# Optimization experiments

Measured on AMD Instinct MI355X. Metric: run time of the kernel, lower is better.

## Reference

```python
import jax, jax.numpy as jnp
import numpy as np

V, M, E, H = 20000, 32, 128, 4      # vocab, max news per word, embed dim, heads
N, L, C = 8192, 64, 128             # num news, max sent len, cnn out channels
KS = (3, 4, 5)


def setup_inputs() -> dict:
    key = jax.random.key(0)
    ks = jax.random.split(key, 12)
    s = 0.02
    return {
        "word2news": jax.random.randint(ks[0], (V, M), 0, N),
        "word2news_len": jax.random.randint(ks[1], (V,), 0, M),
        "news_words": jax.random.randint(ks[2], (N, L), 0, V),
        "news_embed_table": jax.random.normal(ks[3], (N, E), jnp.float32) * s,
        "in_proj_w": jax.random.normal(ks[4], (3 * E, E), jnp.float32) * s,
        "in_proj_b": jnp.zeros((3 * E,), jnp.float32),
        "out_proj_w": jax.random.normal(ks[5], (E, E), jnp.float32) * s,
        "out_proj_b": jnp.zeros((E,), jnp.float32),
        "conv_w3": jax.random.normal(ks[6], (C, E, 3), jnp.float32) * s,
        "conv_b3": jnp.zeros((C,), jnp.float32),
        "conv_w4": jax.random.normal(ks[7], (C, E, 4), jnp.float32) * s,
        "conv_b4": jnp.zeros((C,), jnp.float32),
        "conv_w5": jax.random.normal(ks[8], (C, E, 5), jnp.float32) * s,
        "conv_b5": jnp.zeros((C,), jnp.float32),
        "fc_w": jax.random.normal(ks[9], (E, len(KS) * C), jnp.float32) * s,
        "fc_b": jnp.zeros((E,), jnp.float32),
    }


def _conv1d(x, w, b):
    # x: [N, E, L]  w: [C, E, k]  -> [N, C, L-k+1]
    y = jax.lax.conv_general_dilated(x, w, (1,), "VALID",
                                     dimension_numbers=("NCH", "OIH", "NCH"))
    return y + b[None, :, None]


def _word_embeds(word2news, word2news_len, table, in_w, in_b, out_w, out_b):
    # Batched version of the per-word loop: masked mean query + 1-query MHA.
    mask = jnp.arange(M)[None, :] < word2news_len[:, None]          # [V, M]
    ctx = table[word2news]                                           # [V, M, E]
    cnt = jnp.maximum(word2news_len, 1).astype(ctx.dtype)[:, None]
    q = jnp.sum(jnp.where(mask[:, :, None], ctx, 0.0), axis=1) / cnt  # [V, E]
    wq, wk, wv = jnp.split(in_w, 3, axis=0)
    bq, bk, bv = jnp.split(in_b, 3, axis=0)
    Dh = E // H
    qh = (q @ wq.T + bq).reshape(V, H, Dh)
    kh = (ctx @ wk.T + bk).reshape(V, M, H, Dh)
    vh = (ctx @ wv.T + bv).reshape(V, M, H, Dh)
    scores = jnp.einsum("vhd,vmhd->vhm", qh, kh) / jnp.sqrt(jnp.asarray(Dh, ctx.dtype))
    scores = jnp.where(mask[:, None, :], scores, -1e9)
    attn = jax.nn.softmax(scores, axis=-1)
    o = jnp.einsum("vhm,vmhd->vhd", attn, vh).reshape(V, E)
    o = o @ out_w.T + out_b
    # words with no news stay zero, matching the zeros-init table in torch
    return jnp.where((word2news_len > 0)[:, None], o, 0.0)            # [V, E]


def reference(word2news, word2news_len, news_words, news_embed_table,
              in_proj_w, in_proj_b, out_proj_w, out_proj_b,
              conv_w3, conv_b3, conv_w4, conv_b4, conv_w5, conv_b5,
              fc_w, fc_b):
    word_embeds = _word_embeds(word2news, word2news_len, news_embed_table,
                               in_proj_w, in_proj_b, out_proj_w, out_proj_b)
    doc = word_embeds[news_words]                 # [N, L, E]
    x = doc.transpose(0, 2, 1)                    # [N, E, L]
    pooled = [jnp.max(jax.nn.relu(_conv1d(x, w, b)), axis=2)
              for w, b in ((conv_w3, conv_b3), (conv_w4, conv_b4), (conv_w5, conv_b5))]
    feats = jnp.concatenate(pooled, axis=1)       # [N, 3*C]; dropout=identity (eval)
    return feats @ fc_w.T + fc_b                  # [N, E]
```

## Files before the change

kernel.cpp:

```cpp
#include <hip/hip_runtime.h>
#include <math.h>

#define V_WORDS 20000
#define MM 32
#define EE 128
#define HH 4
#define DHH 32
#define NN 8192
#define LL 64
#define CC 128

typedef short bf16x8 __attribute__((ext_vector_type(8)));
typedef float f32x4 __attribute__((ext_vector_type(4)));
typedef unsigned short u16;
typedef unsigned int u32;

__device__ __forceinline__ u16 f2bf(float x) {
    u32 u = __float_as_uint(x);
    u32 r = (u + 0x7FFFu + ((u >> 16) & 1u)) >> 16;
    return (u16)r;
}
__device__ __forceinline__ float bflo(u32 u) { return __uint_as_float(u << 16); }
__device__ __forceinline__ float bfhi(u32 u) { return __uint_as_float(u & 0xFFFF0000u); }

#if defined(__has_builtin)
#  if __has_builtin(__builtin_amdgcn_fdot2_f32_bf16)
#    define USE_BF16_DOT2 1
#  endif
#endif
#ifdef USE_BF16_DOT2
typedef __bf16 v2bf __attribute__((ext_vector_type(2)));
#endif

__device__ __forceinline__ float dot2bf(u32 a, u32 b, float c) {
#ifdef USE_BF16_DOT2
    return __builtin_amdgcn_fdot2_f32_bf16(
        __builtin_bit_cast(v2bf, a), __builtin_bit_cast(v2bf, b), c, false);
#else
    return c + bflo(a) * bflo(b) + bfhi(a) * bfhi(b);
#endif
}

__global__ __launch_bounds__(256)
void pack_weights(const float* __restrict__ w3,
                  const float* __restrict__ w4,
                  const float* __restrict__ w5,
                  u16* __restrict__ Bpack)
{
    const int s = blockIdx.x;
    const int t = threadIdx.x;
    const int lane = t & 63;

    const float* src;
    int K, sl;
    if (s < 12)      { src = w3; K = 3; sl = s; }
    else if (s < 28) { src = w4; K = 4; sl = s - 12; }
    else             { src = w5; K = 5; sl = s - 28; }
    const int j  = sl >> 2;
    const int e0 = (sl & 3) * 32;

    for (int nt = (t >> 6); nt < 8; nt += 4) {
        const int c = nt * 16 + (lane & 15);
        const int kb = (lane >> 4) * 8;
        u16 vals[8];
        #pragma unroll
        for (int i = 0; i < 8; ++i) {
            const int e = e0 + kb + i;
            vals[i] = f2bf(src[(c * EE + e) * K + j]);
        }
        u16* dst = Bpack + (((size_t)s * 8 + nt) * 64 + lane) * 8;
        *(bf16x8*)dst = *(const bf16x8*)vals;
    }
}

__global__ __launch_bounds__(256)
void kv_proj_kernel(const float* __restrict__ table,
                    const float* __restrict__ in_w,
                    const float* __restrict__ in_b,
                    u16* __restrict__ Kn16, u16* __restrict__ Vn16)
{
    const int n0 = blockIdx.x * 8;
    const int t = threadIdx.x;
    __shared__ float tbl[8][EE];
    {
        const int r = t >> 5, q4 = (t & 31) * 4;
        *(float4*)&tbl[r][q4] = *(const float4*)&table[(size_t)(n0 + r) * EE + q4];
    }
    __syncthreads();

    const int sel = t >> 7;
    const int i = t & 127;
    const float* w = in_w + (size_t)(sel + 1) * EE * EE + (size_t)i * EE;
    const float bias = in_b[(sel + 1) * EE + i];

    float acc[8];
    #pragma unroll
    for (int r = 0; r < 8; ++r) acc[r] = bias;
    for (int k = 0; k < EE; k += 4) {
        const float4 wv = *(const float4*)&w[k];
        #pragma unroll
        for (int r = 0; r < 8; ++r) {
            acc[r] += tbl[r][k]     * wv.x + tbl[r][k + 1] * wv.y
                    + tbl[r][k + 2] * wv.z + tbl[r][k + 3] * wv.w;
        }
    }
    u16* dst = sel ? Vn16 : Kn16;
    #pragma unroll
    for (int r = 0; r < 8; ++r) dst[(size_t)(n0 + r) * EE + i] = f2bf(acc[r]);
}

__global__ __launch_bounds__(384)
void kvqw_proj_kernel(const float* __restrict__ table,
                      const float* __restrict__ in_w,
                      const float* __restrict__ in_b,
                      const float* __restrict__ out_w,
                      const float* __restrict__ out_b,
                      u16* __restrict__ Qn16,
                      u16* __restrict__ Kn16,
                      u16* __restrict__ Wn16)
{
    const int n0 = blockIdx.x * 8;
    const int t = threadIdx.x;
    __shared__ float tbl[8][EE];
    __shared__ float vsh[8][EE];
    if (t < 256) {
        const int r = t >> 5, q4 = (t & 31) * 4;
        *(float4*)&tbl[r][q4] = *(const float4*)&table[(size_t)(n0 + r) * EE + q4];
    }
    __syncthreads();

    const int sel = t >> 7;
    const int i = t & 127;
    const float* w = in_w + (size_t)sel * EE * EE + (size_t)i * EE;
    const float bias = in_b[sel * EE + i];

    float acc[8];
    #pragma unroll
    for (int r = 0; r < 8; ++r) acc[r] = bias;
    for (int k = 0; k < EE; k += 4) {
        const float4 wv = *(const float4*)&w[k];
        #pragma unroll
        for (int r = 0; r < 8; ++r) {
            acc[r] += tbl[r][k]     * wv.x + tbl[r][k + 1] * wv.y
                    + tbl[r][k + 2] * wv.z + tbl[r][k + 3] * wv.w;
        }
    }
    if (sel == 0) {
        #pragma unroll
        for (int r = 0; r < 8; ++r) Qn16[(size_t)(n0 + r) * EE + i] = f2bf(acc[r]);
    } else if (sel == 1) {
        #pragma unroll
        for (int r = 0; r < 8; ++r) Kn16[(size_t)(n0 + r) * EE + i] = f2bf(acc[r]);
    } else {
        #pragma unroll
        for (int r = 0; r < 8; ++r) vsh[r][i] = acc[r];
    }
    __syncthreads();

    {
        const int g = t >> 7;
        const int r0 = g, r1 = g + 3, r2 = g + 6;
        const int r2c = (r2 < 8) ? r2 : 7;
        const float* wr = out_w + (size_t)i * EE;
        const float ob = out_b[i];
        float a0 = ob, a1 = ob, a2 = ob;
        #pragma unroll 4
        for (int k = 0; k < EE; k += 4) {
            const float4 wv = *(const float4*)&wr[k];
            a0 += vsh[r0][k]   * wv.x + vsh[r0][k+1] * wv.y
                + vsh[r0][k+2] * wv.z + vsh[r0][k+3] * wv.w;
            a1 += vsh[r1][k]   * wv.x + vsh[r1][k+1] * wv.y
                + vsh[r1][k+2] * wv.z + vsh[r1][k+3] * wv.w;
            a2 += vsh[r2c][k]   * wv.x + vsh[r2c][k+1] * wv.y
                + vsh[r2c][k+2] * wv.z + vsh[r2c][k+3] * wv.w;
        }
        Wn16[(size_t)(n0 + r0) * EE + i] = f2bf(a0);
        Wn16[(size_t)(n0 + r1) * EE + i] = f2bf(a1);
        if (r2 < 8) Wn16[(size_t)(n0 + r2) * EE + i] = f2bf(a2);
    }
}

#define WPB 8
__global__ __launch_bounds__(256, 3)
void word_attn_kernel(const int* __restrict__ word2news,
                      const int* __restrict__ word2news_len,
                      const float* __restrict__ table,
                      const float* __restrict__ in_w,
                      const float* __restrict__ in_b,
                      const float* __restrict__ out_w,
                      const float* __restrict__ out_b,
                      const u16* __restrict__ Kn16,
                      const u16* __restrict__ Vn16,
                      u16* __restrict__ we16)
{
    const int v0 = blockIdx.x * WPB;
    const int t = threadIdx.x;

    __shared__ int   rows[WPB][MM];
    __shared__ int   lenS[WPB];
    __shared__ float q[WPB][EE];
    __shared__ float qh[WPB][EE];
    __shared__ float attn[WPB][HH][MM];
    __shared__ float osh[WPB][EE];

    {
        const int w = t >> 5, m = t & 31;
        rows[w][m] = word2news[(size_t)(v0 + w) * MM + m];
        if (t < WPB) lenS[t] = word2news_len[v0 + t];
    }
    __syncthreads();

    {
        const int w = t >> 5, d0 = (t & 31) * 4;
        const int L = lenS[w];
        float4 a = {0.f, 0.f, 0.f, 0.f};
        #pragma unroll 4
        for (int m = 0; m < MM; ++m) {
            const float4 x = *(const float4*)&table[(size_t)rows[w][m] * EE + d0];
            if (m < L) { a.x += x.x; a.y += x.y; a.z += x.z; a.w += x.w; }
        }
        const float inv = (L > 0) ? 1.0f / (float)L : 0.0f;
        a.x *= inv; a.y *= inv; a.z *= inv; a.w *= inv;
        *(float4*)&q[w][d0] = a;
    }
    __syncthreads();

    {
        const int g = t >> 7, i = t & 127;
        const float* wr = in_w + (size_t)i * EE;
        float acc[4] = {0.f, 0.f, 0.f, 0.f};
        #pragma unroll 4
        for (int k = 0; k < EE; k += 4) {
            const float4 wv = *(const float4*)&wr[k];
            #pragma unroll
            for (int w4 = 0; w4 < 4; ++w4) {
                const float* qw = q[g * 4 + w4];
                acc[w4] += qw[k] * wv.x + qw[k + 1] * wv.y
                         + qw[k + 2] * wv.z + qw[k + 3] * wv.w;
            }
        }
        const float b = in_b[i];
        #pragma unroll
        for (int w4 = 0; w4 < 4; ++w4) qh[g * 4 + w4][i] = acc[w4] + b;
    }
    __syncthreads();

    {
        const int w = t >> 5, m = t & 31;
        const int L = lenS[w];
        float s[HH] = {-1e9f, -1e9f, -1e9f, -1e9f};
        if (m < L) {
            const uint4* kr = (const uint4*)(Kn16 + (size_t)rows[w][m] * EE);
            #pragma unroll 1
            for (int h = 0; h < HH; ++h) {
                float a = 0.f;
                #pragma unroll
                for (int k8 = 0; k8 < 4; ++k8) {
                    const uint4 u = kr[h * 4 + k8];
                    const float4 q0 = *(const float4*)&qh[w][h * 32 + k8 * 8];
                    const float4 q1 = *(const float4*)&qh[w][h * 32 + k8 * 8 + 4];
                    a += q0.x * bflo(u.x) + q0.y * bfhi(u.x)
                       + q0.z * bflo(u.y) + q0.w * bfhi(u.y)
                       + q1.x * bflo(u.z) + q1.y * bfhi(u.z)
                       + q1.z * bflo(u.w) + q1.w * bfhi(u.w);
                }
                s[h] = a * 0.17677669529663687f;
            }
        }
        #pragma unroll
        for (int h = 0; h < HH; ++h) {
            float mx = s[h];
            #pragma unroll
            for (int off = 16; off > 0; off >>= 1)
                mx = fmaxf(mx, __shfl_xor(mx, off, 32));
            const float ex = expf(s[h] - mx);
            float sum = ex;
            #pragma unroll
            for (int off = 16; off > 0; off >>= 1)
                sum += __shfl_xor(sum, off, 32);
            attn[w][h][m] = ex / sum;
        }
    }
    __syncthreads();

    {
        const int w = t >> 5, d0 = (t & 31) * 4;
        const int h = d0 >> 5;
        float4 a = {0.f, 0.f, 0.f, 0.f};
        #pragma unroll 4
        for (int m = 0; m < MM; ++m) {
            const float aw = attn[w][h][m];
            const u32* vr = (const u32*)(Vn16 + (size_t)rows[w][m] * EE + d0);
            const u32 u0 = vr[0], u1 = vr[1];
            a.x += aw * bflo(u0); a.y += aw * bfhi(u0);
            a.z += aw * bflo(u1); a.w += aw * bfhi(u1);
        }
        *(float4*)&osh[w][d0] = a;
    }
    __syncthreads();

    {
        const int g = t >> 7, i = t & 127;
        const float* wr = out_w + (size_t)i * EE;
        float acc[4] = {0.f, 0.f, 0.f, 0.f};
        #pragma unroll 4
        for (int k = 0; k < EE; k += 4) {
            const float4 wv = *(const float4*)&wr[k];
            #pragma unroll
            for (int w4 = 0; w4 < 4; ++w4) {
                const float* ow = osh[g * 4 + w4];
                acc[w4] += ow[k] * wv.x + ow[k + 1] * wv.y
                         + ow[k + 2] * wv.z + ow[k + 3] * wv.w;
            }
        }
        const float b = out_b[i];
        #pragma unroll
        for (int w4 = 0; w4 < 4; ++w4) {
            const int w = g * 4 + w4;
            we16[(size_t)(v0 + w) * EE + i] =
                (lenS[w] > 0) ? f2bf(acc[w4] + b) : (u16)0;
        }
    }
}

__global__ __launch_bounds__(256, 3)
void word_attn_wn(const int* __restrict__ word2news,
                  const int* __restrict__ word2news_len,
                  const u16* __restrict__ Qn16,
                  const u16* __restrict__ Kn16,
                  const u16* __restrict__ Wn16,
                  u16* __restrict__ we16)
{
    const int v0 = blockIdx.x * WPB;
    const int t = threadIdx.x;

    __shared__ int   rows[WPB][MM];
    __shared__ int   lenS[WPB];
    __shared__ __align__(16) u32 qhp[WPB][EE / 2];
    __shared__ float attn[WPB][HH][MM];

    {
        const int w = t >> 5, m = t & 31;
        rows[w][m] = word2news[(size_t)(v0 + w) * MM + m];
        if (t < WPB) lenS[t] = word2news_len[v0 + t];
    }
    __syncthreads();

    {
        const int w = t >> 5, d0 = (t & 31) * 4;
        const int L = lenS[w];
        float4 a = {0.f, 0.f, 0.f, 0.f};
        #pragma unroll 4
        for (int m = 0; m < L; ++m) {
            const uint2 u = *(const uint2*)(Qn16 + (size_t)rows[w][m] * EE + d0);
            a.x += bflo(u.x); a.y += bfhi(u.x);
            a.z += bflo(u.y); a.w += bfhi(u.y);
        }
        const float inv = (L > 0) ? 1.0f / (float)L : 0.0f;
        a.x *= inv; a.y *= inv; a.z *= inv; a.w *= inv;
        qhp[w][(d0 >> 1) + 0] = (u32)f2bf(a.x) | ((u32)f2bf(a.y) << 16);
        qhp[w][(d0 >> 1) + 1] = (u32)f2bf(a.z) | ((u32)f2bf(a.w) << 16);
    }
    __syncthreads();

    {
        const int w = t >> 5, m = t & 31;
        const int L = lenS[w];
        float s[HH] = {-1e9f, -1e9f, -1e9f, -1e9f};
        if (m < L) {
            const uint4* kr = (const uint4*)(Kn16 + (size_t)rows[w][m] * EE);
            const u32* qp = qhp[w];
            #pragma unroll
            for (int hp = 0; hp < 2; ++hp) {
                uint4 kq[8];
                #pragma unroll
                for (int q8 = 0; q8 < 8; ++q8) kq[q8] = kr[hp * 8 + q8];
                #pragma unroll
                for (int hl = 0; hl < 2; ++hl) {
                    const int h = hp * 2 + hl;
                    float a = 0.f;
                    #pragma unroll
                    for (int k8 = 0; k8 < 4; ++k8) {
                        const uint4 u  = kq[hl * 4 + k8];
                        const uint4 qq = *(const uint4*)&qp[h * 16 + k8 * 4];
                        a = dot2bf(u.x, qq.x, a);
                        a = dot2bf(u.y, qq.y, a);
                        a = dot2bf(u.z, qq.z, a);
                        a = dot2bf(u.w, qq.w, a);
                    }
                    s[h] = a * 0.17677669529663687f;
                }
            }
        }
        #pragma unroll
        for (int h = 0; h < HH; ++h) {
            float mx = s[h];
            #pragma unroll
            for (int off = 16; off > 0; off >>= 1)
                mx = fmaxf(mx, __shfl_xor(mx, off, 32));
            const float ex = expf(s[h] - mx);
            float sum = ex;
            #pragma unroll
            for (int off = 16; off > 0; off >>= 1)
                sum += __shfl_xor(sum, off, 32);
            attn[w][h][m] = ex / sum;
        }
    }
    __syncthreads();

    {
        const int w = t >> 5, d0 = (t & 31) * 4;
        const int h = d0 >> 5;
        const int L = lenS[w];
        float4 a = {0.f, 0.f, 0.f, 0.f};
        #pragma unroll 4
        for (int m = 0; m < L; ++m) {
            const float aw = attn[w][h][m];
            const uint2 u = *(const uint2*)(Wn16 + (size_t)rows[w][m] * EE + d0);
            a.x += aw * bflo(u.x); a.y += aw * bfhi(u.x);
            a.z += aw * bflo(u.y); a.w += aw * bfhi(u.y);
        }
        u32 lo = 0u, hi = 0u;
        if (L > 0) {
            lo = (u32)f2bf(a.x) | ((u32)f2bf(a.y) << 16);
            hi = (u32)f2bf(a.z) | ((u32)f2bf(a.w) << 16);
        }
        u32* dst = (u32*)(we16 + (size_t)(v0 + w) * EE + d0);
        dst[0] = lo; dst[1] = hi;
    }
}

#define DSTRIDE 136
#define DOCSZ   (68 * DSTRIDE)

template<int NSL, int SBASE, int NP>
__device__ __forceinline__ void conv_g2(const u16* __restrict__ lds,
                                        const u16* __restrict__ Bpack,
                                        const float* __restrict__ bk,
                                        int p, int nth, int l,
                                        float (&mxout)[4])
{
    f32x4 acc[4][4];
    #pragma unroll
    for (int mt = 0; mt < 4; ++mt)
        #pragma unroll
        for (int k = 0; k < 4; ++k)
            acc[mt][k] = (f32x4){0.f, 0.f, 0.f, 0.f};

    const int lm = l & 15;
    const int g  = l >> 4;
    const u16* bbase = Bpack + ((size_t)SBASE * 8 + nth * 4) * 512 + l * 8;
    const u16* abase = lds + (size_t)p * DOCSZ;

    #pragma unroll 2
    for (int s = 0; s < NSL; ++s) {
        const int j  = s >> 2;
        const int e0 = (s & 3) * 32;

        bf16x8 b[4];
        #pragma unroll
        for (int k = 0; k < 4; ++k)
            b[k] = *(const bf16x8*)(bbase + s * 4096 + k * 512);

        const u16* arow = abase + (lm + j) * DSTRIDE + e0 + g * 8;
        bf16x8 a[4];
        #pragma unroll
        for (int mt = 0; mt < 4; ++mt)
            a[mt] = *(const bf16x8*)(arow + mt * (16 * DSTRIDE));

        #pragma unroll
        for (int mt = 0; mt < 4; ++mt)
            #pragma unroll
            for (int k = 0; k < 4; ++k)
                acc[mt][k] = __builtin_amdgcn_mfma_f32_16x16x32_bf16(a[mt], b[k], acc[mt][k], 0, 0, 0);
    }

    #pragma unroll
    for (int k = 0; k < 4; ++k) {
        const int c = nth * 64 + k * 16 + lm;
        const float bias = bk[c];
        float mx = 0.0f;
        #pragma unroll
        for (int mt = 0; mt < 4; ++mt) {
            #pragma unroll
            for (int r = 0; r < 4; ++r) {
                const int pos = 16 * mt + g * 4 + r;
                const float y = fmaxf(acc[mt][k][r] + bias, 0.0f);
                if (pos < NP) mx = fmaxf(mx, y);
            }
        }
        mx = fmaxf(mx, __shfl_xor(mx, 16));
        mx = fmaxf(mx, __shfl_xor(mx, 32));
        mxout[k] = mx;
    }
}

__global__ __launch_bounds__(512, 4)
void news_kernel(const int* __restrict__ news_words,
                 const u16* __restrict__ we16,
                 const u16* __restrict__ Bpack,
                 const float* __restrict__ b3,
                 const float* __restrict__ b4,
                 const float* __restrict__ b5,
                 const float* __restrict__ fcw, const float* __restrict__ fcb,
                 float* __restrict__ out)
{
    const int n0 = blockIdx.x * 4;
    const int t = threadIdx.x;
    const int w = t >> 6, l = t & 63;
    const int p = w >> 1, nth = w & 1;

    __shared__ u16 lds[4 * DOCSZ];
    __shared__ int rows[4 * LL];

    if (t < 4 * LL) rows[t] = news_words[(size_t)n0 * LL + t];
    __syncthreads();

    {
        const uint4* weU = (const uint4*)we16;
        uint4* ldsU = (uint4*)lds;
        for (int idx = t; idx < 4096; idx += 512) {
            const int d = idx >> 10, rem = idx & 1023;
            const int row = rem >> 4, c4 = rem & 15;
            ldsU[d * 1156 + row * 17 + c4] = weU[(size_t)rows[d * 64 + row] * 16 + c4];
        }
        if (t < 256) {
            const int d = t >> 6, rem = t & 63;
            const int row = 64 + (rem >> 4), c4 = rem & 15;
            ldsU[d * 1156 + row * 17 + c4] = (uint4){0u, 0u, 0u, 0u};
        }
    }
    __syncthreads();

    float m3[4], m4[4], m5[4];
    conv_g2<12,  0, 62>(lds, Bpack, b3, p, nth, l, m3);
    conv_g2<16, 12, 61>(lds, Bpack, b4, p, nth, l, m4);
    conv_g2<20, 28, 60>(lds, Bpack, b5, p, nth, l, m5);
    __syncthreads();

    float* feats = (float*)lds;
    if ((l >> 4) == 0) {
        const int lm = l & 15;
        #pragma unroll
        for (int k = 0; k < 4; ++k) {
            const int c = nth * 64 + k * 16 + lm;
            feats[p * 384 +   0 + c] = m3[k];
            feats[p * 384 + 128 + c] = m4[k];
            feats[p * 384 + 256 + c] = m5[k];
        }
    }
    __syncthreads();

    if (t < 128) {
        const float4* wr4 = (const float4*)(fcw + (size_t)t * (3 * CC));
        float a0 = fcb[t], a1 = a0, a2 = a0, a3 = a0;
        for (int f4 = 0; f4 < 96; ++f4) {
            const float4 wv = wr4[f4];
            const float4 x0 = *(const float4*)&feats[0 * 384 + f4 * 4];
            const float4 x1 = *(const float4*)&feats[1 * 384 + f4 * 4];
            const float4 x2 = *(const float4*)&feats[2 * 384 + f4 * 4];
            const float4 x3 = *(const float4*)&feats[3 * 384 + f4 * 4];
            a0 += x0.x * wv.x + x0.y * wv.y + x0.z * wv.z + x0.w * wv.w;
            a1 += x1.x * wv.x + x1.y * wv.y + x1.z * wv.z + x1.w * wv.w;
            a2 += x2.x * wv.x + x2.y * wv.y + x2.z * wv.z + x2.w * wv.w;
            a3 += x3.x * wv.x + x3.y * wv.y + x3.z * wv.z + x3.w * wv.w;
        }
        out[(size_t)(n0 + 0) * EE + t] = a0;
        out[(size_t)(n0 + 1) * EE + t] = a1;
        out[(size_t)(n0 + 2) * EE + t] = a2;
        out[(size_t)(n0 + 3) * EE + t] = a3;
    }
}

extern "C" void kernel_launch(void* const* d_in, const int* in_sizes, int n_in,
                              void* d_out, int out_size, void* d_ws, size_t ws_size,
                              hipStream_t stream)
{
    const int*   word2news     = (const int*)d_in[0];
    const int*   word2news_len = (const int*)d_in[1];
    const int*   news_words    = (const int*)d_in[2];
    const float* table         = (const float*)d_in[3];
    const float* in_w          = (const float*)d_in[4];
    const float* in_b          = (const float*)d_in[5];
    const float* out_w         = (const float*)d_in[6];
    const float* out_b         = (const float*)d_in[7];
    const float* w3            = (const float*)d_in[8];
    const float* b3            = (const float*)d_in[9];
    const float* w4            = (const float*)d_in[10];
    const float* b4            = (const float*)d_in[11];
    const float* w5            = (const float*)d_in[12];
    const float* b5            = (const float*)d_in[13];
    const float* fcw           = (const float*)d_in[14];
    const float* fcb           = (const float*)d_in[15];

    float* out = (float*)d_out;
    u16* base  = (u16*)d_ws;
    u16* we16  = base;
    u16* Bpack = base + 2560000;
    u16* Kn16  = base + 2756608;
    u16* Wn16  = base + 3805184;
    u16* Qn16  = base + 4853760;
    const size_t need_qn = (size_t)(4853760 + 1048576) * 2;

    pack_weights<<<48, 256, 0, stream>>>(w3, w4, w5, Bpack);

    if (ws_size >= need_qn) {
        kvqw_proj_kernel<<<NN / 8, 384, 0, stream>>>(table, in_w, in_b,
                                                     out_w, out_b,
                                                     Qn16, Kn16, Wn16);
        word_attn_wn<<<V_WORDS / WPB, 256, 0, stream>>>(
            word2news, word2news_len, Qn16, Kn16, Wn16, we16);
    } else {
        kv_proj_kernel<<<NN / 8, 256, 0, stream>>>(table, in_w, in_b, Kn16, Wn16);
        word_attn_kernel<<<V_WORDS / WPB, 256, 0, stream>>>(
            word2news, word2news_len, table, in_w, in_b, out_w, out_b,
            Kn16, Wn16, we16);
    }

    news_kernel<<<NN / 4, 512, 0, stream>>>(
        news_words, we16, Bpack, b3, b4, b5, fcw, fcb, out);
}
```

Baseline: 364.5 us.

## Assign 64 threads per word in attention kernel, splitting rows and heads

```diff
diff --git a/kernel.cpp b/kernel.cpp
--- a/kernel.cpp
+++ b/kernel.cpp
@@ -323,6 +323,7 @@
     }
 }
 
+#define WPW 4
 __global__ __launch_bounds__(256, 3)
 void word_attn_wn(const int* __restrict__ word2news,
                   const int* __restrict__ word2news_len,
@@ -331,102 +332,114 @@
                   const u16* __restrict__ Wn16,
                   u16* __restrict__ we16)
 {
-    const int v0 = blockIdx.x * WPB;
+    const int v0 = blockIdx.x * WPW;
     const int t = threadIdx.x;
-
-    __shared__ int   rows[WPB][MM];
-    __shared__ int   lenS[WPB];
-    __shared__ __align__(16) u32 qhp[WPB][EE / 2];
-    __shared__ float attn[WPB][HH][MM];
-
-    {
-        const int w = t >> 5, m = t & 31;
-        rows[w][m] = word2news[(size_t)(v0 + w) * MM + m];
-        if (t < WPB) lenS[t] = word2news_len[v0 + t];
-    }
-    __syncthreads();
-
-    {
-        const int w = t >> 5, d0 = (t & 31) * 4;
-        const int L = lenS[w];
+    const int w   = t >> 6;
+    const int l   = t & 63;
+    const int h2  = l >> 5;
+    const int m32 = l & 31;
+
+    __shared__ int   rows[WPW][MM];
+    __shared__ int   lenS[WPW];
+    __shared__ __align__(16) u32 qhp[WPW][EE / 2];
+    __shared__ float attn[WPW][HH][MM];
+
+    {
+        if (t < WPW * MM) rows[t >> 5][t & 31] = word2news[(size_t)v0 * MM + t];
+        if (t < WPW) lenS[t] = word2news_len[v0 + t];
+    }
+    __syncthreads();
+
+    const int L  = lenS[w];
+    const int d0 = m32 * 4;
+
+    {
         float4 a = {0.f, 0.f, 0.f, 0.f};
         #pragma unroll 4
-        for (int m = 0; m < L; ++m) {
-            const uint2 u = *(const uint2*)(Qn16 + (size_t)rows[w][m] * EE + d0);
-            a.x += bflo(u.x); a.y += bfhi(u.x);
-            a.z += bflo(u.y); a.w += bfhi(u.y);
-        }
+        for (int mm = 0; mm < L; mm += 2) {
+            const int ri = mm + h2;
+            if (ri < L) {
+                const uint2 u = *(const uint2*)(Qn16 + (size_t)rows[w][ri] * EE + d0);
+                a.x += bflo(u.x); a.y += bfhi(u.x);
+                a.z += bflo(u.y); a.w += bfhi(u.y);
+            }
+        }
+        a.x += __shfl_xor(a.x, 32);
+        a.y += __shfl_xor(a.y, 32);
+        a.z += __shfl_xor(a.z, 32);
+        a.w += __shfl_xor(a.w, 32);
         const float inv = (L > 0) ? 1.0f / (float)L : 0.0f;
-        a.x *= inv; a.y *= inv; a.z *= inv; a.w *= inv;
-        qhp[w][(d0 >> 1) + 0] = (u32)f2bf(a.x) | ((u32)f2bf(a.y) << 16);
-        qhp[w][(d0 >> 1) + 1] = (u32)f2bf(a.z) | ((u32)f2bf(a.w) << 16);
-    }
-    __syncthreads();
-
-    {
-        const int w = t >> 5, m = t & 31;
-        const int L = lenS[w];
-        float s[HH] = {-1e9f, -1e9f, -1e9f, -1e9f};
-        if (m < L) {
-            const uint4* kr = (const uint4*)(Kn16 + (size_t)rows[w][m] * EE);
+        if (h2 == 0) {
+            qhp[w][(d0 >> 1) + 0] = (u32)f2bf(a.x * inv) | ((u32)f2bf(a.y * inv) << 16);
+            qhp[w][(d0 >> 1) + 1] = (u32)f2bf(a.z * inv) | ((u32)f2bf(a.w * inv) << 16);
+        }
+    }
+    __syncthreads();
+
+    {
+        float s[2] = {-1e9f, -1e9f};
+        if (m32 < L) {
+            const uint4* kr = (const uint4*)(Kn16 + (size_t)rows[w][m32] * EE);
+            uint4 kq[8];
+            #pragma unroll
+            for (int i = 0; i < 8; ++i) kq[i] = kr[h2 * 8 + i];
             const u32* qp = qhp[w];
             #pragma unroll
-            for (int hp = 0; hp < 2; ++hp) {
-                uint4 kq[8];
+            for (int hl = 0; hl < 2; ++hl) {
+                const int h = h2 * 2 + hl;
+                float a = 0.f;
                 #pragma unroll
-                for (int q8 = 0; q8 < 8; ++q8) kq[q8] = kr[hp * 8 + q8];
-                #pragma unroll
-                for (int hl = 0; hl < 2; ++hl) {
-                    const int h = hp * 2 + hl;
-                    float a = 0.f;
-                    #pragma unroll
-                    for (int k8 = 0; k8 < 4; ++k8) {
-                        const uint4 u  = kq[hl * 4 + k8];
-                        const uint4 qq = *(const uint4*)&qp[h * 16 + k8 * 4];
-                        a = dot2bf(u.x, qq.x, a);
-                        a = dot2bf(u.y, qq.y, a);
-                        a = dot2bf(u.z, qq.z, a);
-                        a = dot2bf(u.w, qq.w, a);
-                    }
-                    s[h] = a * 0.17677669529663687f;
+                for (int k8 = 0; k8 < 4; ++k8) {
+                    const uint4 u  = kq[hl * 4 + k8];
+                    const uint4 qq = *(const uint4*)&qp[h * 16 + k8 * 4];
+                    a = dot2bf(u.x, qq.x, a);
+                    a = dot2bf(u.y, qq.y, a);
+                    a = dot2bf(u.z, qq.z, a);
+                    a = dot2bf(u.w, qq.w, a);
                 }
+                s[hl] = a * 0.17677669529663687f;
             }
         }
         #pragma unroll
-        for (int h = 0; h < HH; ++h) {
-            float mx = s[h];
+        for (int hl = 0; hl < 2; ++hl) {
+            float mx = s[hl];
             #pragma unroll
             for (int off = 16; off > 0; off >>= 1)
                 mx = fmaxf(mx, __shfl_xor(mx, off, 32));
-            const float ex = expf(s[h] - mx);
+            const float ex = __expf(s[hl] - mx);
             float sum = ex;
             #pragma unroll
             for (int off = 16; off > 0; off >>= 1)
                 sum += __shfl_xor(sum, off, 32);
-            attn[w][h][m] = ex / sum;
-        }
-    }
-    __syncthreads();
-
-    {
-        const int w = t >> 5, d0 = (t & 31) * 4;
-        const int h = d0 >> 5;
-        const int L = lenS[w];
+            attn[w][h2 * 2 + hl][m32] = ex / sum;
+        }
+    }
+    __syncthreads();
+
+    {
+        const int h = m32 >> 3;
         float4 a = {0.f, 0.f, 0.f, 0.f};
         #pragma unroll 4
-        for (int m = 0; m < L; ++m) {
-            const float aw = attn[w][h][m];
-            const uint2 u = *(const uint2*)(Wn16 + (size_t)rows[w][m] * EE + d0);
+        for (int mm = 0; mm < L; mm += 2) {
+            const int ri = mm + h2;
+            const float aw = attn[w][h][ri];
+            const uint2 u = *(const uint2*)(Wn16 + (size_t)rows[w][ri] * EE + d0);
             a.x += aw * bflo(u.x); a.y += aw * bfhi(u.x);
             a.z += aw * bflo(u.y); a.w += aw * bfhi(u.y);
         }
-        u32 lo = 0u, hi = 0u;
-        if (L > 0) {
-            lo = (u32)f2bf(a.x) | ((u32)f2bf(a.y) << 16);
-            hi = (u32)f2bf(a.z) | ((u32)f2bf(a.w) << 16);
-        }
-        u32* dst = (u32*)(we16 + (size_t)(v0 + w) * EE + d0);
-        dst[0] = lo; dst[1] = hi;
+        a.x += __shfl_xor(a.x, 32);
+        a.y += __shfl_xor(a.y, 32);
+        a.z += __shfl_xor(a.z, 32);
+        a.w += __shfl_xor(a.w, 32);
+        if (h2 == 0) {
+            u32 lo = 0u, hi = 0u;
+            if (L > 0) {
+                lo = (u32)f2bf(a.x) | ((u32)f2bf(a.y) << 16);
+                hi = (u32)f2bf(a.z) | ((u32)f2bf(a.w) << 16);
+            }
+            u32* dst = (u32*)(we16 + (size_t)(v0 + w) * EE + d0);
+            dst[0] = lo; dst[1] = hi;
+        }
     }
 }
 
@@ -608,7 +621,7 @@
         kvqw_proj_kernel<<<NN / 8, 384, 0, stream>>>(table, in_w, in_b,
                                                      out_w, out_b,
                                                      Qn16, Kn16, Wn16);
-        word_attn_wn<<<V_WORDS / WPB, 256, 0, stream>>>(
+        word_attn_wn<<<V_WORDS / WPW, 256, 0, stream>>>(
             word2news, word2news_len, Qn16, Kn16, Wn16, we16);
     } else {
         kv_proj_kernel<<<NN / 8, 256, 0, stream>>>(table, in_w, in_b, Kn16, Wn16);
```

Result: slower. 373.0 us (+2.3%).
